# Optimization experiments

Measured on AMD Instinct MI355X. Metric: run time of the kernel, lower is better.

The kernel has to match this reference:

```python
import jax, jax.numpy as jnp
import numpy as np

D_MODEL = 1024
N_HEAD = 16
SEQ = 1024
BATCH = 4
D_K = D_MODEL // N_HEAD
LN_EPS = 1e-6


def setup_inputs() -> dict:
    key = jax.random.key(0)
    ks = jax.random.split(key, 10)
    scale = 1.0 / np.sqrt(D_MODEL)
    return {
        "q": jax.random.normal(ks[0], (SEQ, BATCH, D_MODEL), jnp.float32),
        "k": jax.random.normal(ks[1], (SEQ, BATCH, D_MODEL), jnp.float32),
        "v": jax.random.normal(ks[2], (SEQ, BATCH, D_MODEL), jnp.float32),
        "sph": jax.random.uniform(ks[3], (BATCH, N_HEAD, SEQ, SEQ), jnp.float32),
        "Wq": jax.random.normal(ks[4], (D_MODEL, D_MODEL), jnp.float32) * scale,
        "Wk": jax.random.normal(ks[5], (D_MODEL, D_MODEL), jnp.float32) * scale,
        "Wv": jax.random.normal(ks[6], (D_MODEL, D_MODEL), jnp.float32) * scale,
        "Wo": jax.random.normal(ks[7], (D_MODEL, D_MODEL), jnp.float32) * scale,
        "gamma": jnp.ones((D_MODEL,), jnp.float32),
        "beta": jnp.zeros((D_MODEL,), jnp.float32),
    }


def reference(q, k, v, sph, Wq, Wk, Wv, Wo, gamma, beta):
    # q,k,v: [S, B, D] -> batch-first [B, S, D]
    qb = jnp.swapaxes(q, 0, 1)
    kb = jnp.swapaxes(k, 0, 1)
    vb = jnp.swapaxes(v, 0, 1)
    B, S, D = qb.shape
    residual = qb
    # projections (nn.Linear: y = x @ W.T), split heads -> [B, H, S, d_k]
    qh = (qb @ Wq.T).reshape(B, S, N_HEAD, D_K).transpose(0, 2, 1, 3)
    kh = (kb @ Wk.T).reshape(B, S, N_HEAD, D_K).transpose(0, 2, 1, 3)
    vh = (vb @ Wv.T).reshape(B, S, N_HEAD, D_K).transpose(0, 2, 1, 3)
    temp = jnp.float32(np.sqrt(D_K))
    # attention logits with spatial modulation
    attn = jnp.einsum("bhqd,bhkd->bhqk", qh / temp, kh) * sph
    p_attn = jax.nn.softmax(attn, axis=-1)  # dropout = identity (eval)
    out = jnp.einsum("bhqk,bhkd->bhqd", p_attn, vh)
    out = out.transpose(0, 2, 1, 3).reshape(B, S, D)
    out = out @ Wo.T + residual
    # LayerNorm over last dim, eps=1e-6
    mu = jnp.mean(out, axis=-1, keepdims=True)
    var = jnp.var(out, axis=-1, keepdims=True)
    out = (out - mu) * jax.lax.rsqrt(var + LN_EPS) * gamma + beta
    return jnp.swapaxes(out, 0, 1), p_attn
```

## Files before the change

### kernel.cpp

```cpp
#include <hip/hip_runtime.h>
#include <hip/hip_bf16.h>
#include <hip/hip_fp16.h>
#include <cstdint>

constexpr int B_ = 4, H_ = 16, S_ = 1024, D_ = 1024, DK_ = 64;

typedef __bf16 bf16x8 __attribute__((ext_vector_type(8)));
typedef float f32x4 __attribute__((ext_vector_type(4)));
#define MFMA16(a, b, c) __builtin_amdgcn_mfma_f32_16x16x32_bf16(a, b, c, 0, 0, 0)

static __device__ inline unsigned short f2bf(float f) {
  __hip_bfloat16 h = __float2bfloat16(f);
  return *reinterpret_cast<unsigned short*>(&h);
}
static __device__ inline unsigned packbf(float lo, float hi) {
  return ((unsigned)f2bf(hi) << 16) | (unsigned)f2bf(lo);
}
static __device__ inline unsigned pack_f16(float x, float y) {
  __half hx = __float2half(x), hy = __float2half(y);
  return ((unsigned)(*reinterpret_cast<unsigned short*>(&hy)) << 16) |
         (unsigned)(*reinterpret_cast<unsigned short*>(&hx));
}
static __device__ inline float f16lo(unsigned u) {
  unsigned short s = (unsigned short)(u & 0xffff);
  return __half2float(*reinterpret_cast<__half*>(&s));
}
static __device__ inline float f16hi(unsigned u) {
  unsigned short s = (unsigned short)(u >> 16);
  return __half2float(*reinterpret_cast<__half*>(&s));
}

__global__ __launch_bounds__(256) void k_cvt3(const float* __restrict__ x0,
                                              const float* __restrict__ x1,
                                              const float* __restrict__ x2,
                                              __hip_bfloat16* __restrict__ y0,
                                              __hip_bfloat16* __restrict__ y1,
                                              __hip_bfloat16* __restrict__ y2) {
  const int sel = blockIdx.x >> 12;
  const int i = (blockIdx.x & 4095) * 256 + threadIdx.x;
  const float* x = sel == 0 ? x0 : (sel == 1 ? x1 : x2);
  __hip_bfloat16* y = sel == 0 ? y0 : (sel == 1 ? y1 : y2);
  const float4 v = reinterpret_cast<const float4*>(x)[i];
  ushort4 o;
  o.x = f2bf(v.x); o.y = f2bf(v.y); o.z = f2bf(v.z); o.w = f2bf(v.w);
  *reinterpret_cast<ushort4*>(&y[(size_t)i * 4]) = o;
}

__global__ __launch_bounds__(256) void k_cvt4(const float* __restrict__ x0,
                                              const float* __restrict__ x1,
                                              const float* __restrict__ x2,
                                              const float* __restrict__ x3,
                                              __hip_bfloat16* __restrict__ y0,
                                              __hip_bfloat16* __restrict__ y1,
                                              __hip_bfloat16* __restrict__ y2,
                                              __hip_bfloat16* __restrict__ y3) {
  const int sel = blockIdx.x >> 10;
  const int i = (blockIdx.x & 1023) * 256 + threadIdx.x;
  const float* x = sel == 0 ? x0 : (sel == 1 ? x1 : (sel == 2 ? x2 : x3));
  __hip_bfloat16* y = sel == 0 ? y0 : (sel == 1 ? y1 : (sel == 2 ? y2 : y3));
  const float4 v = reinterpret_cast<const float4*>(x)[i];
  ushort4 o;
  o.x = f2bf(v.x); o.y = f2bf(v.y); o.z = f2bf(v.z); o.w = f2bf(v.w);
  *reinterpret_cast<ushort4*>(&y[(size_t)i * 4]) = o;
}

template <int MODE>
__global__ __launch_bounds__(256) void k_gemm(const __hip_bfloat16* __restrict__ A,
                                              const __hip_bfloat16* __restrict__ Bw,
                                              const float* __restrict__ resid,
                                              __hip_bfloat16* __restrict__ Yb,
                                              float* __restrict__ Yf) {
  __shared__ __hip_bfloat16 Als[128 * 64];
  __shared__ __hip_bfloat16 Bls[64 * 64];
  const int tid = threadIdx.x;
  const int lane = tid & 63;
  const int l15 = lane & 15, g = lane >> 4;
  const int w = tid >> 6;
  const int wr = w >> 1, wc = w & 1;
  const int rt = blockIdx.x, ct = blockIdx.y;
  f32x4 acc[4][2] = {};

  for (int k0 = 0; k0 < D_; k0 += 64) {
#pragma unroll
    for (int q = 0; q < 4; ++q) {
      const int slot0 = q * 256 + (tid & 192);
      const int slot = slot0 + lane;
      const int r = slot >> 3, p = slot & 7;
      const int lc = p ^ (r & 7);
      const __hip_bfloat16* src = A + (size_t)(rt * 128 + r) * D_ + k0 + lc * 8;
      __builtin_amdgcn_global_load_lds(
          (const __attribute__((address_space(1))) unsigned int*)src,
          (__attribute__((address_space(3))) unsigned int*)&Als[slot0 * 8], 16, 0, 0);
    }
#pragma unroll
    for (int q = 0; q < 2; ++q) {
      const int slot0 = q * 256 + (tid & 192);
      const int slot = slot0 + lane;
      const int r = slot >> 3, p = slot & 7;
      const int lc = p ^ (r & 7);
      const __hip_bfloat16* src = Bw + (size_t)(ct * 64 + r) * D_ + k0 + lc * 8;
      __builtin_amdgcn_global_load_lds(
          (const __attribute__((address_space(1))) unsigned int*)src,
          (__attribute__((address_space(3))) unsigned int*)&Bls[slot0 * 8], 16, 0, 0);
    }
    __syncthreads();
#pragma unroll
    for (int ks = 0; ks < 2; ++ks) {
      bf16x8 bfr[2];
#pragma unroll
      for (int cf = 0; cf < 2; ++cf) {
        const int r = wc * 32 + cf * 16 + l15;
        const int p = (ks * 4 + g) ^ (r & 7);
        bfr[cf] = *reinterpret_cast<const bf16x8*>(&Bls[(r * 8 + p) * 8]);
      }
#pragma unroll
      for (int fi = 0; fi < 4; ++fi) {
        const int r = wr * 64 + fi * 16 + l15;
        const int p = (ks * 4 + g) ^ (r & 7);
        const bf16x8 af = *reinterpret_cast<const bf16x8*>(&Als[(r * 8 + p) * 8]);
        acc[fi][0] = MFMA16(af, bfr[0], acc[fi][0]);
        acc[fi][1] = MFMA16(af, bfr[1], acc[fi][1]);
      }
    }
    __syncthreads();
  }
#pragma unroll
  for (int fi = 0; fi < 4; ++fi)
#pragma unroll
    for (int cf = 0; cf < 2; ++cf)
#pragma unroll
      for (int r = 0; r < 4; ++r) {
        const int m = rt * 128 + wr * 64 + fi * 16 + 4 * g + r;
        const int t = wc * 32 + cf * 16 + l15;
        const float val = acc[fi][cf][r];
        if (MODE == 0) {
          const int s = m >> 2, b = m & 3;
          Yb[((size_t)((b * H_ + ct) * S_ + s)) * DK_ + t] = __float2bfloat16(val);
        } else if (MODE == 1) {
          const int s = m >> 2, b = m & 3;
          Yb[((size_t)((b * H_ + ct) * DK_ + t)) * S_ + s] = __float2bfloat16(val);
        } else {
          const int b = m >> 10, s = m & 1023;
          const int o = ct * 64 + t;
          Yf[(size_t)m * D_ + o] = val + resid[(size_t)(s * B_ + b) * D_ + o];
        }
      }
}

__global__ __launch_bounds__(256, 4) void k_attn(const __hip_bfloat16* __restrict__ Qh,
                                                 const __hip_bfloat16* __restrict__ Kh,
                                                 const __hip_bfloat16* __restrict__ VT,
                                                 const float* __restrict__ sph,
                                                 float* __restrict__ Pout,
                                                 __hip_bfloat16* __restrict__ O) {
  __shared__ unsigned int Plds[16 * 512];
  __shared__ float sphl[4][1024];
  const int tid = threadIdx.x, lane = tid & 63, w = tid >> 6;
  const int l15 = lane & 15, g = lane >> 4;
  const int it = blockIdx.x, bh = blockIdx.y;
  const unsigned sw = (unsigned)((l15 & 7) << 2);
  const int wrow = w * 4;
  constexpr float kScale = 0.125f * 1.44269504088896f;

  auto dma_row = [&](int rr) {
    const float* src = sph + ((size_t)bh << 20) +
                       (((size_t)(it * 16 + wrow + rr)) << 10) + lane * 4;
#pragma unroll
    for (int i = 0; i < 4; ++i)
      __builtin_amdgcn_global_load_lds(
          (const __attribute__((address_space(1))) unsigned int*)(src + i * 256),
          (__attribute__((address_space(3))) unsigned int*)&sphl[w][i * 256], 16, 0, 0);
  };

  dma_row(0);

  {
    const __hip_bfloat16* qp = Qh + ((size_t)bh * S_ + it * 16 + l15) * DK_ + 8 * g;
    const bf16x8 qf0 = *reinterpret_cast<const bf16x8*>(qp);
    const bf16x8 qf1 = *reinterpret_cast<const bf16x8*>(qp + 32);
    const __hip_bfloat16* kb0 =
        Kh + (size_t)bh * S_ * DK_ + (size_t)(w * 256 + l15) * DK_ + 8 * g;
    bf16x8 kra[2], krb[2], krc[2], krd[2];
    kra[0] = *reinterpret_cast<const bf16x8*>(kb0);
    krb[0] = *reinterpret_cast<const bf16x8*>(kb0 + 32);
    krc[0] = *reinterpret_cast<const bf16x8*>(kb0 + 16 * DK_);
    krd[0] = *reinterpret_cast<const bf16x8*>(kb0 + 16 * DK_ + 32);
#pragma unroll
    for (int j = 0; j < 8; ++j) {
      const int cur = j & 1, nxt = cur ^ 1;
      if (j < 7) {
        const __hip_bfloat16* kp = kb0 + (size_t)(j + 1) * 32 * DK_;
        kra[nxt] = *reinterpret_cast<const bf16x8*>(kp);
        krb[nxt] = *reinterpret_cast<const bf16x8*>(kp + 32);
        krc[nxt] = *reinterpret_cast<const bf16x8*>(kp + 16 * DK_);
        krd[nxt] = *reinterpret_cast<const bf16x8*>(kp + 16 * DK_ + 32);
      }
      f32x4 a0 = {0.f, 0.f, 0.f, 0.f};
      f32x4 a1 = {0.f, 0.f, 0.f, 0.f};
      __builtin_amdgcn_s_setprio(1);
      a0 = MFMA16(kra[cur], qf0, a0);
      a0 = MFMA16(krb[cur], qf1, a0);
      a1 = MFMA16(krc[cur], qf0, a1);
      a1 = MFMA16(krd[cur], qf1, a1);
      __builtin_amdgcn_s_setprio(0);
      const int key0 = w * 256 + j * 32;
      uint2 u0, u1;
      u0.x = pack_f16(a0[0] * kScale, a0[1] * kScale);
      u0.y = pack_f16(a0[2] * kScale, a0[3] * kScale);
      u1.x = pack_f16(a1[0] * kScale, a1[1] * kScale);
      u1.y = pack_f16(a1[2] * kScale, a1[3] * kScale);
      const int base0 = l15 * 512 + (key0 >> 1) + 2 * g;
      *reinterpret_cast<uint2*>(&Plds[(unsigned)base0 ^ sw]) = u0;
      *reinterpret_cast<uint2*>(&Plds[(unsigned)(base0 + 8) ^ sw]) = u1;
    }
  }
  __syncthreads();

#pragma unroll
  for (int rr = 0; rr < 4; ++rr) {
    if (rr > 0) {
      asm volatile("s_waitcnt vmcnt(0)" ::: "memory");
      __builtin_amdgcn_sched_barrier(0);
    }
    const int row = wrow + rr;
    float4 sv[4];
#pragma unroll
    for (int i = 0; i < 4; ++i)
      sv[i] = reinterpret_cast<const float4*>(&sphl[w][0])[lane + 64 * i];
    const unsigned rsw = (unsigned)((row & 7) << 2);
    const int lbase = row * 512;
    uint2 uv[4];
#pragma unroll
    for (int i = 0; i < 4; ++i)
      uv[i] = *reinterpret_cast<uint2*>(
          &Plds[(unsigned)(lbase + 2 * lane + 128 * i) ^ rsw]);
    float va[16];
#pragma unroll
    for (int i = 0; i < 4; ++i) {
      va[4 * i + 0] = f16lo(uv[i].x) * sv[i].x;
      va[4 * i + 1] = f16hi(uv[i].x) * sv[i].y;
      va[4 * i + 2] = f16lo(uv[i].y) * sv[i].z;
      va[4 * i + 3] = f16hi(uv[i].y) * sv[i].w;
    }
    if (rr < 3) dma_row(rr + 1);
    float m = va[0];
#pragma unroll
    for (int i = 1; i < 16; ++i) m = fmaxf(m, va[i]);
#pragma unroll
    for (int off = 1; off < 64; off <<= 1) m = fmaxf(m, __shfl_xor(m, off));
    float sum = 0.f;
#pragma unroll
    for (int i = 0; i < 16; ++i) {
      va[i] = exp2f(va[i] - m);
      sum += va[i];
    }
#pragma unroll
    for (int off = 1; off < 64; off <<= 1) sum += __shfl_xor(sum, off);
    const float inv = 1.f / sum;
    float4* po = reinterpret_cast<float4*>(Pout + ((size_t)bh << 20) +
                                           (((size_t)(it * 16 + row)) << 10));
#pragma unroll
    for (int i = 0; i < 4; ++i) {
      float4 p;
      p.x = va[4 * i + 0] * inv;
      p.y = va[4 * i + 1] * inv;
      p.z = va[4 * i + 2] * inv;
      p.w = va[4 * i + 3] * inv;
      po[lane + 64 * i] = p;
      uint2 pb;
      pb.x = packbf(p.x, p.y);
      pb.y = packbf(p.z, p.w);
      *reinterpret_cast<uint2*>(
          &Plds[(unsigned)(lbase + 2 * lane + 128 * i) ^ rsw]) = pb;
    }
  }
  __syncthreads();

  {
    const int c0 = w * 16;
    f32x4 o0 = {0.f, 0.f, 0.f, 0.f};
    const __hip_bfloat16* vb =
        VT + (size_t)bh * DK_ * S_ + (size_t)(c0 + l15) * S_ + 8 * g;
#pragma unroll
    for (int kb2 = 0; kb2 < 4; ++kb2) {
      bf16x8 vreg[8];
      bf16x8 preg[8];
#pragma unroll
      for (int u = 0; u < 8; ++u)
        vreg[u] = *reinterpret_cast<const bf16x8*>(vb + kb2 * 256 + u * 32);
#pragma unroll
      for (int u = 0; u < 8; ++u) {
        const int k0 = kb2 * 256 + u * 32;
        preg[u] = *reinterpret_cast<const bf16x8*>(
            &Plds[(unsigned)(l15 * 512 + (k0 >> 1) + 4 * g) ^ sw]);
      }
      __builtin_amdgcn_s_setprio(1);
#pragma unroll
      for (int u = 0; u < 8; ++u) o0 = MFMA16(preg[u], vreg[u], o0);
      __builtin_amdgcn_s_setprio(0);
    }
    const int b = bh >> 4, h = bh & 15;
#pragma unroll
    for (int r = 0; r < 4; ++r) {
      const int srow = it * 16 + 4 * g + r;
      O[((size_t)(b * S_ + srow)) * D_ + h * DK_ + c0 + l15] = __float2bfloat16(o0[r]);
    }
  }
}

__global__ __launch_bounds__(256) void k_ln(const float* __restrict__ Z,
                                            const float* __restrict__ gamma,
                                            const float* __restrict__ beta,
                                            float* __restrict__ out) {
  const int r = blockIdx.x;
  const int b = r >> 10, s = r & 1023;
  const int tid = threadIdx.x;
  const float4 z = *reinterpret_cast<const float4*>(Z + (size_t)r * D_ + (tid << 2));
  float sum = z.x + z.y + z.z + z.w;
  float sq = z.x * z.x + z.y * z.y + z.z * z.z + z.w * z.w;
#pragma unroll
  for (int off = 1; off < 64; off <<= 1) {
    sum += __shfl_xor(sum, off);
    sq += __shfl_xor(sq, off);
  }
  __shared__ float rs[4];
  __shared__ float rq[4];
  const int wv = tid >> 6, ln = tid & 63;
  if (ln == 0) { rs[wv] = sum; rq[wv] = sq; }
  __syncthreads();
  const float tsum = rs[0] + rs[1] + rs[2] + rs[3];
  const float tsq = rq[0] + rq[1] + rq[2] + rq[3];
  const float mu = tsum * (1.0f / 1024.0f);
  const float var = tsq * (1.0f / 1024.0f) - mu * mu;
  const float rstd = rsqrtf(var + 1e-6f);
  const float4 gm = *reinterpret_cast<const float4*>(gamma + (tid << 2));
  const float4 bt = *reinterpret_cast<const float4*>(beta + (tid << 2));
  float4 o;
  o.x = (z.x - mu) * rstd * gm.x + bt.x;
  o.y = (z.y - mu) * rstd * gm.y + bt.y;
  o.z = (z.z - mu) * rstd * gm.z + bt.z;
  o.w = (z.w - mu) * rstd * gm.w + bt.w;
  *reinterpret_cast<float4*>(out + (size_t)(s * B_ + b) * D_ + (tid << 2)) = o;
}

extern "C" void kernel_launch(void* const* d_in, const int* in_sizes, int n_in,
                              void* d_out, int out_size, void* d_ws, size_t ws_size,
                              hipStream_t stream) {
  const float* q = (const float*)d_in[0];
  const float* k = (const float*)d_in[1];
  const float* v = (const float*)d_in[2];
  const float* sph = (const float*)d_in[3];
  const float* Wq = (const float*)d_in[4];
  const float* Wk = (const float*)d_in[5];
  const float* Wv = (const float*)d_in[6];
  const float* Wo = (const float*)d_in[7];
  const float* gamma = (const float*)d_in[8];
  const float* beta = (const float*)d_in[9];

  float* out = (float*)d_out;
  float* P = out + (size_t)4 * 1024 * 1024;

  char* ws = (char*)d_ws;
  __hip_bfloat16* xq = (__hip_bfloat16*)(ws);
  __hip_bfloat16* xk = (__hip_bfloat16*)(ws + ((size_t)8 << 20));
  __hip_bfloat16* xv = (__hip_bfloat16*)(ws + ((size_t)16 << 20));
  __hip_bfloat16* wqb = (__hip_bfloat16*)(ws + ((size_t)24 << 20));
  __hip_bfloat16* wkb = (__hip_bfloat16*)(ws + ((size_t)26 << 20));
  __hip_bfloat16* wvb = (__hip_bfloat16*)(ws + ((size_t)28 << 20));
  __hip_bfloat16* wob = (__hip_bfloat16*)(ws + ((size_t)30 << 20));
  __hip_bfloat16* Qh = (__hip_bfloat16*)(ws + ((size_t)32 << 20));
  __hip_bfloat16* Khb = (__hip_bfloat16*)(ws + ((size_t)40 << 20));
  __hip_bfloat16* VTb = (__hip_bfloat16*)(ws + ((size_t)48 << 20));
  __hip_bfloat16* Ob = (__hip_bfloat16*)(ws + ((size_t)56 << 20));
  float* Z = (float*)(ws + ((size_t)64 << 20));

  const dim3 blk(256);
  k_cvt3<<<12288, blk, 0, stream>>>(q, k, v, xq, xk, xv);
  k_cvt4<<<4096, blk, 0, stream>>>(Wq, Wk, Wv, Wo, wqb, wkb, wvb, wob);

  k_gemm<0><<<dim3(32, 16), blk, 0, stream>>>(xq, wqb, nullptr, Qh, nullptr);
  k_gemm<0><<<dim3(32, 16), blk, 0, stream>>>(xk, wkb, nullptr, Khb, nullptr);
  k_gemm<1><<<dim3(32, 16), blk, 0, stream>>>(xv, wvb, nullptr, VTb, nullptr);

  k_attn<<<dim3(64, 64), blk, 0, stream>>>(Qh, Khb, VTb, sph, P, Ob);

  k_gemm<2><<<dim3(32, 16), blk, 0, stream>>>(Ob, wob, q, nullptr, Z);
  k_ln<<<4096, blk, 0, stream>>>(Z, gamma, beta, out);
}
```

Baseline: 284.7 us.

## Widen GEMM tiles to 128x128 and batch softmax rows with direct sph loads

The GEMM kernel now computes 128x128 output tiles instead of 128x64, halving the grid and doubling reuse of each A tile; the epilogue derives head and column indices from the global column. Separately, the attention softmax drops the LDS DMA staging of sph rows, loads sph straight from global memory, and processes all four rows per wave together with interleaved max/sum shuffle reductions for more ILP. The changes raise register pressure (16 accumulators per wave, 64 softmax values per lane), and the GEMM grid shrinks to 256 blocks, which may underfill the GPU's CUs.

```diff
diff --git a/kernel.cpp b/kernel.cpp
--- a/kernel.cpp
+++ b/kernel.cpp
@@ -71,14 +71,14 @@
                                               __hip_bfloat16* __restrict__ Yb,
                                               float* __restrict__ Yf) {
   __shared__ __hip_bfloat16 Als[128 * 64];
-  __shared__ __hip_bfloat16 Bls[64 * 64];
+  __shared__ __hip_bfloat16 Bls[128 * 64];
   const int tid = threadIdx.x;
   const int lane = tid & 63;
   const int l15 = lane & 15, g = lane >> 4;
   const int w = tid >> 6;
   const int wr = w >> 1, wc = w & 1;
   const int rt = blockIdx.x, ct = blockIdx.y;
-  f32x4 acc[4][2] = {};
+  f32x4 acc[4][4] = {};
 
   for (int k0 = 0; k0 < D_; k0 += 64) {
 #pragma unroll
@@ -93,12 +93,12 @@
           (__attribute__((address_space(3))) unsigned int*)&Als[slot0 * 8], 16, 0, 0);
     }
 #pragma unroll
-    for (int q = 0; q < 2; ++q) {
+    for (int q = 0; q < 4; ++q) {
       const int slot0 = q * 256 + (tid & 192);
       const int slot = slot0 + lane;
       const int r = slot >> 3, p = slot & 7;
       const int lc = p ^ (r & 7);
-      const __hip_bfloat16* src = Bw + (size_t)(ct * 64 + r) * D_ + k0 + lc * 8;
+      const __hip_bfloat16* src = Bw + (size_t)(ct * 128 + r) * D_ + k0 + lc * 8;
       __builtin_amdgcn_global_load_lds(
           (const __attribute__((address_space(1))) unsigned int*)src,
           (__attribute__((address_space(3))) unsigned int*)&Bls[slot0 * 8], 16, 0, 0);
@@ -106,10 +106,10 @@
     __syncthreads();
 #pragma unroll
     for (int ks = 0; ks < 2; ++ks) {
-      bf16x8 bfr[2];
-#pragma unroll
-      for (int cf = 0; cf < 2; ++cf) {
-        const int r = wc * 32 + cf * 16 + l15;
+      bf16x8 bfr[4];
+#pragma unroll
+      for (int cf = 0; cf < 4; ++cf) {
+        const int r = wc * 64 + cf * 16 + l15;
         const int p = (ks * 4 + g) ^ (r & 7);
         bfr[cf] = *reinterpret_cast<const bf16x8*>(&Bls[(r * 8 + p) * 8]);
       }
@@ -118,8 +118,8 @@
         const int r = wr * 64 + fi * 16 + l15;
         const int p = (ks * 4 + g) ^ (r & 7);
         const bf16x8 af = *reinterpret_cast<const bf16x8*>(&Als[(r * 8 + p) * 8]);
-        acc[fi][0] = MFMA16(af, bfr[0], acc[fi][0]);
-        acc[fi][1] = MFMA16(af, bfr[1], acc[fi][1]);
+#pragma unroll
+        for (int cf = 0; cf < 4; ++cf) acc[fi][cf] = MFMA16(af, bfr[cf], acc[fi][cf]);
       }
     }
     __syncthreads();
@@ -127,22 +127,23 @@
 #pragma unroll
   for (int fi = 0; fi < 4; ++fi)
 #pragma unroll
-    for (int cf = 0; cf < 2; ++cf)
+    for (int cf = 0; cf < 4; ++cf)
 #pragma unroll
       for (int r = 0; r < 4; ++r) {
         const int m = rt * 128 + wr * 64 + fi * 16 + 4 * g + r;
-        const int t = wc * 32 + cf * 16 + l15;
+        const int tcol = ct * 128 + wc * 64 + cf * 16 + l15;
         const float val = acc[fi][cf][r];
         if (MODE == 0) {
           const int s = m >> 2, b = m & 3;
-          Yb[((size_t)((b * H_ + ct) * S_ + s)) * DK_ + t] = __float2bfloat16(val);
+          const int head = tcol >> 6, dk = tcol & 63;
+          Yb[((size_t)((b * H_ + head) * S_ + s)) * DK_ + dk] = __float2bfloat16(val);
         } else if (MODE == 1) {
           const int s = m >> 2, b = m & 3;
-          Yb[((size_t)((b * H_ + ct) * DK_ + t)) * S_ + s] = __float2bfloat16(val);
+          const int head = tcol >> 6, dk = tcol & 63;
+          Yb[((size_t)((b * H_ + head) * DK_ + dk)) * S_ + s] = __float2bfloat16(val);
         } else {
           const int b = m >> 10, s = m & 1023;
-          const int o = ct * 64 + t;
-          Yf[(size_t)m * D_ + o] = val + resid[(size_t)(s * B_ + b) * D_ + o];
+          Yf[(size_t)m * D_ + tcol] = val + resid[(size_t)(s * B_ + b) * D_ + tcol];
         }
       }
 }
@@ -154,25 +155,12 @@
                                                  float* __restrict__ Pout,
                                                  __hip_bfloat16* __restrict__ O) {
   __shared__ unsigned int Plds[16 * 512];
-  __shared__ float sphl[4][1024];
   const int tid = threadIdx.x, lane = tid & 63, w = tid >> 6;
   const int l15 = lane & 15, g = lane >> 4;
   const int it = blockIdx.x, bh = blockIdx.y;
   const unsigned sw = (unsigned)((l15 & 7) << 2);
   const int wrow = w * 4;
   constexpr float kScale = 0.125f * 1.44269504088896f;
-
-  auto dma_row = [&](int rr) {
-    const float* src = sph + ((size_t)bh << 20) +
-                       (((size_t)(it * 16 + wrow + rr)) << 10) + lane * 4;
-#pragma unroll
-    for (int i = 0; i < 4; ++i)
-      __builtin_amdgcn_global_load_lds(
-          (const __attribute__((address_space(1))) unsigned int*)(src + i * 256),
-          (__attribute__((address_space(3))) unsigned int*)&sphl[w][i * 256], 16, 0, 0);
-  };
-
-  dma_row(0);
 
   {
     const __hip_bfloat16* qp = Qh + ((size_t)bh * S_ + it * 16 + l15) * DK_ + 8 * g;
@@ -216,62 +204,103 @@
   }
   __syncthreads();
 
-#pragma unroll
-  for (int rr = 0; rr < 4; ++rr) {
-    if (rr > 0) {
-      asm volatile("s_waitcnt vmcnt(0)" ::: "memory");
-      __builtin_amdgcn_sched_barrier(0);
-    }
-    const int row = wrow + rr;
-    float4 sv[4];
-#pragma unroll
-    for (int i = 0; i < 4; ++i)
-      sv[i] = reinterpret_cast<const float4*>(&sphl[w][0])[lane + 64 * i];
-    const unsigned rsw = (unsigned)((row & 7) << 2);
-    const int lbase = row * 512;
-    uint2 uv[4];
-#pragma unroll
-    for (int i = 0; i < 4; ++i)
-      uv[i] = *reinterpret_cast<uint2*>(
-          &Plds[(unsigned)(lbase + 2 * lane + 128 * i) ^ rsw]);
-    float va[16];
-#pragma unroll
-    for (int i = 0; i < 4; ++i) {
-      va[4 * i + 0] = f16lo(uv[i].x) * sv[i].x;
-      va[4 * i + 1] = f16hi(uv[i].x) * sv[i].y;
-      va[4 * i + 2] = f16lo(uv[i].y) * sv[i].z;
-      va[4 * i + 3] = f16hi(uv[i].y) * sv[i].w;
-    }
-    if (rr < 3) dma_row(rr + 1);
-    float m = va[0];
-#pragma unroll
-    for (int i = 1; i < 16; ++i) m = fmaxf(m, va[i]);
-#pragma unroll
-    for (int off = 1; off < 64; off <<= 1) m = fmaxf(m, __shfl_xor(m, off));
-    float sum = 0.f;
-#pragma unroll
-    for (int i = 0; i < 16; ++i) {
-      va[i] = exp2f(va[i] - m);
-      sum += va[i];
-    }
-#pragma unroll
-    for (int off = 1; off < 64; off <<= 1) sum += __shfl_xor(sum, off);
-    const float inv = 1.f / sum;
-    float4* po = reinterpret_cast<float4*>(Pout + ((size_t)bh << 20) +
-                                           (((size_t)(it * 16 + row)) << 10));
-#pragma unroll
-    for (int i = 0; i < 4; ++i) {
-      float4 p;
-      p.x = va[4 * i + 0] * inv;
-      p.y = va[4 * i + 1] * inv;
-      p.z = va[4 * i + 2] * inv;
-      p.w = va[4 * i + 3] * inv;
-      po[lane + 64 * i] = p;
-      uint2 pb;
-      pb.x = packbf(p.x, p.y);
-      pb.y = packbf(p.z, p.w);
-      *reinterpret_cast<uint2*>(
-          &Plds[(unsigned)(lbase + 2 * lane + 128 * i) ^ rsw]) = pb;
+  {
+    const float4* sbase = reinterpret_cast<const float4*>(
+        sph + ((size_t)bh << 20) + (((size_t)(it * 16)) << 10));
+    float va[4][16];
+    float m4[4], s4[4];
+#pragma unroll
+    for (int rr = 0; rr < 4; ++rr) {
+      const int row = wrow + rr;
+      const unsigned rsw = (unsigned)((row & 7) << 2);
+      const int lbase = row * 512;
+      uint2 uv[4];
+      float4 sv[4];
+#pragma unroll
+      for (int i = 0; i < 4; ++i) {
+        sv[i] = sbase[(size_t)row * 256 + lane + 64 * i];
+        uv[i] = *reinterpret_cast<uint2*>(
+            &Plds[(unsigned)(lbase + 2 * lane + 128 * i) ^ rsw]);
+      }
+#pragma unroll
+      for (int i = 0; i < 4; ++i) {
+        va[rr][4 * i + 0] = f16lo(uv[i].x) * sv[i].x;
+        va[rr][4 * i + 1] = f16hi(uv[i].x) * sv[i].y;
+        va[rr][4 * i + 2] = f16lo(uv[i].y) * sv[i].z;
+        va[rr][4 * i + 3] = f16hi(uv[i].y) * sv[i].w;
+      }
+    }
+#pragma unroll
+    for (int rr = 0; rr < 4; ++rr) {
+      float b0 = fmaxf(va[rr][0], va[rr][1]);
+      float b1 = fmaxf(va[rr][2], va[rr][3]);
+      float b2 = fmaxf(va[rr][4], va[rr][5]);
+      float b3 = fmaxf(va[rr][6], va[rr][7]);
+      float b4 = fmaxf(va[rr][8], va[rr][9]);
+      float b5 = fmaxf(va[rr][10], va[rr][11]);
+      float b6 = fmaxf(va[rr][12], va[rr][13]);
+      float b7 = fmaxf(va[rr][14], va[rr][15]);
+      m4[rr] = fmaxf(fmaxf(fmaxf(b0, b1), fmaxf(b2, b3)),
+                     fmaxf(fmaxf(b4, b5), fmaxf(b6, b7)));
+    }
+#pragma unroll
+    for (int off = 1; off < 64; off <<= 1) {
+      const float t0 = __shfl_xor(m4[0], off);
+      const float t1 = __shfl_xor(m4[1], off);
+      const float t2 = __shfl_xor(m4[2], off);
+      const float t3 = __shfl_xor(m4[3], off);
+      m4[0] = fmaxf(m4[0], t0);
+      m4[1] = fmaxf(m4[1], t1);
+      m4[2] = fmaxf(m4[2], t2);
+      m4[3] = fmaxf(m4[3], t3);
+    }
+#pragma unroll
+    for (int rr = 0; rr < 4; ++rr) {
+#pragma unroll
+      for (int i = 0; i < 16; ++i) va[rr][i] = exp2f(va[rr][i] - m4[rr]);
+      float b0 = va[rr][0] + va[rr][1];
+      float b1 = va[rr][2] + va[rr][3];
+      float b2 = va[rr][4] + va[rr][5];
+      float b3 = va[rr][6] + va[rr][7];
+      float b4 = va[rr][8] + va[rr][9];
+      float b5 = va[rr][10] + va[rr][11];
+      float b6 = va[rr][12] + va[rr][13];
+      float b7 = va[rr][14] + va[rr][15];
+      s4[rr] = ((b0 + b1) + (b2 + b3)) + ((b4 + b5) + (b6 + b7));
+    }
+#pragma unroll
+    for (int off = 1; off < 64; off <<= 1) {
+      const float t0 = __shfl_xor(s4[0], off);
+      const float t1 = __shfl_xor(s4[1], off);
+      const float t2 = __shfl_xor(s4[2], off);
+      const float t3 = __shfl_xor(s4[3], off);
+      s4[0] += t0;
+      s4[1] += t1;
+      s4[2] += t2;
+      s4[3] += t3;
+    }
+#pragma unroll
+    for (int rr = 0; rr < 4; ++rr) {
+      const int row = wrow + rr;
+      const unsigned rsw = (unsigned)((row & 7) << 2);
+      const int lbase = row * 512;
+      const float inv = 1.f / s4[rr];
+      float4* po = reinterpret_cast<float4*>(Pout + ((size_t)bh << 20) +
+                                             (((size_t)(it * 16 + row)) << 10));
+#pragma unroll
+      for (int i = 0; i < 4; ++i) {
+        float4 p;
+        p.x = va[rr][4 * i + 0] * inv;
+        p.y = va[rr][4 * i + 1] * inv;
+        p.z = va[rr][4 * i + 2] * inv;
+        p.w = va[rr][4 * i + 3] * inv;
+        po[lane + 64 * i] = p;
+        uint2 pb;
+        pb.x = packbf(p.x, p.y);
+        pb.y = packbf(p.z, p.w);
+        *reinterpret_cast<uint2*>(
+            &Plds[(unsigned)(lbase + 2 * lane + 128 * i) ^ rsw]) = pb;
+      }
     }
   }
   __syncthreads();
@@ -378,12 +407,12 @@
   k_cvt3<<<12288, blk, 0, stream>>>(q, k, v, xq, xk, xv);
   k_cvt4<<<4096, blk, 0, stream>>>(Wq, Wk, Wv, Wo, wqb, wkb, wvb, wob);
 
-  k_gemm<0><<<dim3(32, 16), blk, 0, stream>>>(xq, wqb, nullptr, Qh, nullptr);
-  k_gemm<0><<<dim3(32, 16), blk, 0, stream>>>(xk, wkb, nullptr, Khb, nullptr);
-  k_gemm<1><<<dim3(32, 16), blk, 0, stream>>>(xv, wvb, nullptr, VTb, nullptr);
+  k_gemm<0><<<dim3(32, 8), blk, 0, stream>>>(xq, wqb, nullptr, Qh, nullptr);
+  k_gemm<0><<<dim3(32, 8), blk, 0, stream>>>(xk, wkb, nullptr, Khb, nullptr);
+  k_gemm<1><<<dim3(32, 8), blk, 0, stream>>>(xv, wvb, nullptr, VTb, nullptr);
 
   k_attn<<<dim3(64, 64), blk, 0, stream>>>(Qh, Khb, VTb, sph, P, Ob);
 
-  k_gemm<2><<<dim3(32, 16), blk, 0, stream>>>(Ob, wob, q, nullptr, Z);
+  k_gemm<2><<<dim3(32, 8), blk, 0, stream>>>(Ob, wob, q, nullptr, Z);
   k_ln<<<4096, blk, 0, stream>>>(Z, gamma, beta, out);
 }
```

Result: slower. 313.0 us (+10.0%).
